# Kernel tuning notes

Hardware: AMD Instinct MI355X
Metric: run time of the kernel (lower is better)

## Reference

```python
import jax, jax.numpy as jnp
import numpy as np

V, K, E, T, B = 30000, 50, 300, 60, 128
TH, H, L = 800, 200, 3
DELTA = 0.005


def setup_inputs():
    key = jax.random.key(0)
    ks = jax.random.split(key, 32)
    n = jax.random.normal
    inp = {}
    inp['bows'] = jax.random.randint(ks[0], (B, V), 0, 5).astype(jnp.float32)
    inp['normalized_bows'] = jax.random.uniform(ks[1], (B, V), jnp.float32)
    inp['times'] = jax.random.randint(ks[2], (B,), 0, T).astype(jnp.int32)
    inp['rnn_inp'] = jax.random.uniform(ks[3], (T, V), jnp.float32)
    inp['num_docs'] = 100000
    inp['eps_alpha'] = n(ks[4], (T, K, E), jnp.float32)
    inp['eps_eta'] = n(ks[5], (T, K), jnp.float32)
    inp['eps_theta'] = n(ks[6], (B, K), jnp.float32)
    # parameters
    inp['rho'] = n(ks[7], (V, E), jnp.float32) * 0.1
    inp['mu_q_alpha'] = n(ks[8], (K, T, E), jnp.float32)
    inp['logsigma_q_alpha'] = n(ks[9], (K, T, E), jnp.float32) * 0.1
    s = lambda d: np.float32(1.0 / np.sqrt(d))
    inp['W1'] = n(ks[10], (TH, V + K), jnp.float32) * s(V + K)
    inp['b1'] = jnp.zeros((TH,), jnp.float32)
    inp['W2'] = n(ks[11], (TH, TH), jnp.float32) * s(TH)
    inp['b2'] = jnp.zeros((TH,), jnp.float32)
    inp['Wmu_t'] = n(ks[12], (K, TH), jnp.float32) * s(TH)
    inp['bmu_t'] = jnp.zeros((K,), jnp.float32)
    inp['Wls_t'] = n(ks[13], (K, TH), jnp.float32) * s(TH)
    inp['bls_t'] = jnp.zeros((K,), jnp.float32)
    inp['Wmap'] = n(ks[14], (H, V), jnp.float32) * s(V)
    inp['bmap'] = jnp.zeros((H,), jnp.float32)
    inp['lstm_Wih'] = n(ks[15], (L, 4 * H, H), jnp.float32) * s(H)
    inp['lstm_Whh'] = n(ks[16], (L, 4 * H, H), jnp.float32) * s(H)
    inp['lstm_bih'] = jnp.zeros((L, 4 * H), jnp.float32)
    inp['lstm_bhh'] = jnp.zeros((L, 4 * H), jnp.float32)
    inp['Wmu_e'] = n(ks[17], (K, H + K), jnp.float32) * s(H + K)
    inp['bmu_e'] = jnp.zeros((K,), jnp.float32)
    inp['Wls_e'] = n(ks[18], (K, H + K), jnp.float32) * s(H + K)
    inp['bls_e'] = jnp.zeros((K,), jnp.float32)
    return inp


def _kl(qm, qls, pm, pls):
    # KL(N(qm, exp(qls)) || N(pm, exp(pls))), summed over last dim (matches torch code)
    return 0.5 * jnp.sum((jnp.exp(qls) + (qm - pm) ** 2) / (jnp.exp(pls) + 1e-6)
                         - 1.0 + pls - qls, axis=-1)


def _lstm_layer(x, Wih, Whh, bih, bhh):
    # x: [T, in]; PyTorch gate order i,f,g,o
    Hh = Whh.shape[1]
    def step(carry, xt):
        h, c = carry
        g = Wih @ xt + bih + Whh @ h + bhh
        i, f, gg, o = jnp.split(g, 4)
        c = jax.nn.sigmoid(f) * c + jax.nn.sigmoid(i) * jnp.tanh(gg)
        h = jax.nn.sigmoid(o) * jnp.tanh(c)
        return (h, c), h
    init = (jnp.zeros((Hh,), x.dtype), jnp.zeros((Hh,), x.dtype))
    _, ys = jax.lax.scan(step, init, x)
    return ys


def reference(bows, normalized_bows, times, rnn_inp, num_docs, eps_alpha, eps_eta,
              eps_theta, rho, mu_q_alpha, logsigma_q_alpha, W1, b1, W2, b2,
              Wmu_t, bmu_t, Wls_t, bls_t, Wmap, bmap, lstm_Wih, lstm_Whh,
              lstm_bih, lstm_bhh, Wmu_e, bmu_e, Wls_e, bls_e):
    nT = mu_q_alpha.shape[1]
    nK = mu_q_alpha.shape[0]
    logdelta = jnp.log(jnp.asarray(DELTA, jnp.float32))
    # ---- get_alpha (vectorized: alphas have no sequential dependence) ----
    mu_a = jnp.transpose(mu_q_alpha, (1, 0, 2))        # [T,K,E]
    ls_a = jnp.transpose(logsigma_q_alpha, (1, 0, 2))  # [T,K,E]
    alphas = mu_a + eps_alpha * jnp.exp(0.5 * ls_a)
    kl_a0 = _kl(mu_a[0], ls_a[0], 0.0, 0.0)                       # [K]
    kl_at = _kl(mu_a[1:], ls_a[1:], alphas[:-1], logdelta)        # [T-1,K]
    kl_alpha = kl_a0.sum() + kl_at.sum()
    # ---- get_eta (sequential chain via scan) ----
    inp_map = rnn_inp @ Wmap.T + bmap                 # [T,H]
    out = inp_map
    for l in range(lstm_Wih.shape[0]):
        out = _lstm_layer(out, lstm_Wih[l], lstm_Whh[l], lstm_bih[l], lstm_bhh[l])
    inp0 = jnp.concatenate([out[0], jnp.zeros((nK,), out.dtype)])
    mu0 = Wmu_e @ inp0 + bmu_e
    ls0 = Wls_e @ inp0 + bls_e
    eta0 = mu0 + eps_eta[0] * jnp.exp(0.5 * ls0)
    kl_e0 = _kl(mu0, ls0, 0.0, 0.0)
    def step(eta_prev, xs):
        out_t, eps_t = xs
        inp_t = jnp.concatenate([out_t, eta_prev])
        mu_t = Wmu_e @ inp_t + bmu_e
        ls_t = Wls_e @ inp_t + bls_e
        eta_t = mu_t + eps_t * jnp.exp(0.5 * ls_t)
        kl_t = _kl(mu_t, ls_t, eta_prev, logdelta)
        return eta_t, (eta_t, kl_t)
    _, (etas_rest, kls) = jax.lax.scan(step, eta0, (out[1:], eps_eta[1:]))
    etas = jnp.concatenate([eta0[None], etas_rest], axis=0)   # [T,K]
    kl_eta = kl_e0 + kls.sum()
    # ---- get_theta ----
    eta_td = etas[times]                                       # [B,K]
    qt_in = jnp.concatenate([normalized_bows, eta_td], axis=1) # [B,V+K]
    h1 = jax.nn.relu(qt_in @ W1.T + b1)
    h2 = jax.nn.relu(h1 @ W2.T + b2)
    mu_th = h2 @ Wmu_t.T + bmu_t
    ls_th = h2 @ Wls_t.T + bls_t
    z = mu_th + eps_theta * jnp.exp(0.5 * ls_th)
    theta = jax.nn.softmax(z, axis=-1)                         # [B,K]
    kl_theta = _kl(mu_th, ls_th, eta_td, 0.0)                  # [B]
    # ---- get_beta / nll ----
    logit = jnp.einsum('tke,ve->tkv', alphas, rho)             # [T,K,V]
    beta = jax.nn.softmax(logit, axis=-1)
    beta_td = beta[times]                                      # [B,K,V]
    loglik = jnp.log(jnp.einsum('bk,bkv->bv', theta, beta_td) + 1e-6)
    nll = (-(loglik * bows)).sum(-1)                           # [B]
    coeff = jnp.asarray(num_docs / bows.shape[0], jnp.float32)
    nll_tot = nll.sum() * coeff
    kl_theta_tot = kl_theta.sum() * coeff
    nelbo = nll_tot + kl_alpha + kl_eta + kl_theta_tot
    return (nelbo, nll_tot, kl_alpha, kl_eta, kl_theta_tot)
```

## Files before the change

### kernel.cpp

```cpp
#include <hip/hip_runtime.h>
#include <hip/hip_fp16.h>
#include <math.h>

#define TID ((int)threadIdx.x)

#define NVB 235
#define NVB2 79

static __device__ __forceinline__ float sigf(float x){ return 1.f/(1.f+expf(-x)); }

static __device__ __forceinline__ unsigned short f2bf(float f){
  unsigned u = __float_as_uint(f);
  unsigned r = (u + 0x7FFFu + ((u>>16)&1u)) >> 16;
  return (unsigned short)r;
}

typedef short v8ss __attribute__((ext_vector_type(8)));
typedef float v16f __attribute__((ext_vector_type(16)));
union I4BF { int4 i; v8ss s; };
union U16B { int4 i; __half2 h2[4]; };

#define REP25(M) M(0) M(1) M(2) M(3) M(4) M(5) M(6) M(7) M(8) M(9) M(10) M(11) \
                 M(12) M(13) M(14) M(15) M(16) M(17) M(18) M(19) M(20) M(21) M(22) M(23) M(24)

#define DECLW(n) int4 w##n = wrow[n];
#define DOTW(n) { U16B u; u.i = w##n; \
    float4 hA = hs4[2*(n)], hB = hs4[2*(n)+1]; \
    float2 q0=__half22float2(u.h2[0]), q1=__half22float2(u.h2[1]); \
    float2 q2=__half22float2(u.h2[2]), q3=__half22float2(u.h2[3]); \
    a0=fmaf(q0.x,hA.x,a0); a1=fmaf(q0.y,hA.y,a1); \
    a2=fmaf(q1.x,hA.z,a2); a3=fmaf(q1.y,hA.w,a3); \
    a0=fmaf(q2.x,hB.x,a0); a1=fmaf(q2.y,hB.y,a1); \
    a2=fmaf(q3.x,hB.z,a2); a3=fmaf(q3.y,hB.w,a3); }

__global__ void k_zero(float* acc, int* flags){
  if (TID<8) acc[TID]=0.f;
  if (TID<160) flags[TID]=0;
}

__global__ void k_alphas(const float* __restrict__ mqa, const float* __restrict__ lqa,
                         const float* __restrict__ eps, float* __restrict__ alphas){
  int i = blockIdx.x*256+TID; if (i>=900000) return;
  int t = i/15000, r = i%15000, k = r/300, e = r%300;
  int src = k*18000 + t*300 + e;
  float mu = mqa[src], ls = lqa[src];
  alphas[i] = mu + eps[i]*expf(0.5f*ls);
}

__global__ void k_klalpha(const float* __restrict__ mqa, const float* __restrict__ lqa,
                          const float* __restrict__ alphas, float* acc){
  __shared__ float red[256];
  int i = blockIdx.x*256+TID;
  float term = 0.f;
  if (i<900000){
    int t = i/15000, r = i%15000, k = r/300, e = r%300;
    int src = k*18000 + t*300 + e;
    float mu = mqa[src], ls = lqa[src];
    if (t==0){
      term = (expf(ls)+mu*mu)*(1.0f/(1.0f+1e-6f)) - 1.f - ls;
    } else {
      float d = mu - alphas[i-15000];
      term = (expf(ls)+d*d)*(1.0f/(0.005f+1e-6f)) - 1.f + logf(0.005f) - ls;
    }
  }
  red[TID]=term; __syncthreads();
  for (int s=128;s>0;s>>=1){ if (TID<s) red[TID]+=red[TID+s]; __syncthreads(); }
  if (TID==0) atomicAdd(acc+0, 0.5f*red[0]);
}

__global__ void k_prep_rho(const float* __restrict__ rho, unsigned short* __restrict__ rho_f){
  int tid = blockIdx.x*256+TID;
  if (tid >= 940*19*64) return;
  int lane = tid & 63;
  int F = tid >> 6;
  int kstep = F % 19;
  int r32 = F / 19;
  int v = r32*32 + (lane & 31);
  int e0 = kstep*16 + ((lane>>5)<<3);
  unsigned short u[8];
  #pragma unroll
  for (int j=0;j<8;j++){
    int e = e0 + j;
    float val = (v < 30000 && e < 300) ? rho[v*300 + e] : 0.f;
    u[j] = f2bf(val);
  }
  int4 o;
  o.x = (int)u[0] | ((int)u[1]<<16);
  o.y = (int)u[2] | ((int)u[3]<<16);
  o.z = (int)u[4] | ((int)u[5]<<16);
  o.w = (int)u[6] | ((int)u[7]<<16);
  ((int4*)rho_f)[tid] = o;
}

__global__ void k_prep_alpha(const float* __restrict__ alphas, unsigned short* __restrict__ alpha_f){
  int tid = blockIdx.x*256+TID;
  if (tid >= 60*2*19*64) return;
  int lane = tid & 63;
  int F = tid >> 6;
  int kstep = F % 19;
  int tn = F / 19;
  int nt = tn % 2, t = tn / 2;
  int k = nt*32 + (lane & 31);
  int e0 = kstep*16 + ((lane>>5)<<3);
  unsigned short u[8];
  #pragma unroll
  for (int j=0;j<8;j++){
    int e = e0 + j;
    float val = (k < 50 && e < 300) ? alphas[t*15000 + k*300 + e] : 0.f;
    u[j] = f2bf(val);
  }
  int4 o;
  o.x = (int)u[0] | ((int)u[1]<<16);
  o.y = (int)u[2] | ((int)u[3]<<16);
  o.z = (int)u[4] | ((int)u[5]<<16);
  o.w = (int)u[6] | ((int)u[7]<<16);
  ((int4*)alpha_f)[tid] = o;
}

__global__ void k_prep_w16(const float* __restrict__ Whh, const float* __restrict__ Wih,
                           __half* __restrict__ WhhH, __half* __restrict__ WihH){
  int i = blockIdx.x*256+TID;
  if (i<480000){
    WhhH[i] = __float2half_rn(Whh[i]);
    WihH[i] = __float2half_rn(Wih[i]);
  }
}

__global__ void k_iminit(float* __restrict__ im, const float* __restrict__ bmap){
  int i = blockIdx.x*256+TID; if (i<12000) im[i] = bmap[i%200];
}

__global__ __launch_bounds__(256,2) void k_imgemm(const float* __restrict__ rnn,
        const float* __restrict__ Wmap, float* __restrict__ im){
  __shared__ __align__(16) float Ws[32*500];
  __shared__ __align__(16) float rnS[500];
  int hb = blockIdx.x;
  int kb = blockIdx.y;
  int h0 = hb*32;
  int nh = (h0+32<=200)?32:(200-h0);
  const int kbase = kb*500;
  for (int i=TID; i<nh*125; i+=256){
    int h = i/125, q = i%125;
    *reinterpret_cast<float4*>(&Ws[h*500 + q*4]) =
      *reinterpret_cast<const float4*>(&Wmap[(h0+h)*30000 + kbase + q*4]);
  }
  int h = TID>>3, sub = TID&7;
  bool act = (h < nh);
  __syncthreads();
  for (int t=0;t<60;t++){
    if (TID<125)
      *reinterpret_cast<float4*>(&rnS[TID*4]) =
        *reinterpret_cast<const float4*>(&rnn[t*30000 + kbase + TID*4]);
    __syncthreads();
    float a = 0.f;
    if (act){
      const float2* wp = reinterpret_cast<const float2*>(&Ws[h*500]);
      const float2* rp = reinterpret_cast<const float2*>(rnS);
      for (int k2=sub;k2<250;k2+=8){
        float2 wv=wp[k2], rv=rp[k2];
        a = fmaf(wv.x,rv.x,a); a = fmaf(wv.y,rv.y,a);
      }
    }
    a += __shfl_down(a,4); a += __shfl_down(a,2); a += __shfl_down(a,1);
    if (act && sub==0) atomicAdd(&im[t*200 + h0 + h], a);
    __syncthreads();
  }
}

__global__ void k_pregates(const float* __restrict__ x, const float* __restrict__ Wih,
                           const float* __restrict__ bih, const float* __restrict__ bhh,
                           float* __restrict__ pre){
  __shared__ float xS[200];
  int t = blockIdx.x;
  if (TID<200) xS[TID] = x[t*200+TID];
  __syncthreads();
  int r = blockIdx.y*256 + TID;
  if (r>=800) return;
  float a = bih[r] + bhh[r];
  const float* wp = Wih + r*200;
  #pragma unroll 4
  for (int c=0;c<200;c++) a = fmaf(wp[c], xS[c], a);
  pre[t*800+r] = a;
}

__global__ void k_h1init(float* __restrict__ h1, const float* __restrict__ b1){
  int i = blockIdx.x*256+TID; if (i<102400) h1[i] = b1[i%800];
}


static __device__ __forceinline__ void pipe_wait(int* flag, int val){
  if (TID==0){
    while (__hip_atomic_load(flag, __ATOMIC_ACQUIRE, __HIP_MEMORY_SCOPE_AGENT) < val)
      __builtin_amdgcn_s_sleep(2);
  }
  __syncthreads();
}

static __device__ __forceinline__ void pipe_post(int* flag, int val){
  if (TID==0)
    __hip_atomic_store(flag, val, __ATOMIC_RELEASE, __HIP_MEMORY_SCOPE_AGENT);
}

static __device__ void lstm_rec(char* sm, const float* __restrict__ pre,
    const __half* __restrict__ WhhH, float* __restrict__ out,
    int* inFlag, int* outFlag)
{
  float* hsF = (float*)sm;
  float* gsh = (float*)(sm + 800);
  __half* wtH = (__half*)(sm + 4000);
  for (int i=TID;i<6400;i+=768) wtH[i] = WhhH[768*200 + i];
  const int4* wrow = reinterpret_cast<const int4*>(WhhH + TID*200);
  REP25(DECLW)
  float c_reg = 0.f;
  if (TID<200) hsF[TID]=0.f;
  int j = TID - 512;
  int trow = (j>=0) ? (j>>3) : 0;
  int tseg = (j>=0) ? (j&7)*25 : 0;
  __syncthreads();
  for (int t=0;t<60;t++){
    if (inFlag) pipe_wait(inFlag, t+1);
    float p = pre[t*800+TID];
    float a0=0.f,a1=0.f,a2=0.f,a3=0.f;
    const float4* hs4 = reinterpret_cast<const float4*>(hsF);
    REP25(DOTW)
    gsh[TID] = a0+a1+a2+a3 + p;
    if (j>=0){
      float pa = 0.f;
      const __half* wt = &wtH[trow*200 + tseg];
      const float* hp = &hsF[tseg];
      #pragma unroll
      for (int c2=0;c2<25;c2++) pa = fmaf(__half2float(wt[c2]), hp[c2], pa);
      pa += __shfl_down(pa,4); pa += __shfl_down(pa,2); pa += __shfl_down(pa,1);
      if ((j&7)==0) gsh[768+trow] = pa + pre[t*800+768+trow];
    }
    __syncthreads();
    if (TID<200){
      float ii=gsh[TID], ff=gsh[200+TID], gg=gsh[400+TID], oo=gsh[600+TID];
      float c = sigf(ff)*c_reg + sigf(ii)*tanhf(gg);
      c_reg = c;
      float h = sigf(oo)*tanhf(c);
      hsF[TID]=h;
      out[t*200+TID]=h;
    }
    __syncthreads();
    if (outFlag) pipe_post(outFlag, t+1);
  }
}

static __device__ void lstm_gemv(char* sm, const float* __restrict__ xIn,
    const __half* __restrict__ WH, const float* __restrict__ bih,
    const float* __restrict__ bhh, float* __restrict__ preOut,
    int* inFlag, int* outFlag)
{
  float* xS = (float*)sm;
  __half* wtG = (__half*)(sm + 800);
  for (int i=TID;i<6400;i+=768) wtG[i] = WH[768*200 + i];
  const int4* wrow = reinterpret_cast<const int4*>(WH + TID*200);
  REP25(DECLW)
  float bb = bih[TID] + bhh[TID];
  int j = TID - 512;
  int trow = (j>=0) ? (j>>3) : 0;
  int tseg = (j>=0) ? (j&7)*25 : 0;
  float bbT = 0.f;
  if (j>=0 && (j&7)==0) bbT = bih[768+trow] + bhh[768+trow];
  for (int t=0;t<60;t++){
    pipe_wait(inFlag, t+1);
    if (TID<200) xS[TID] = xIn[t*200+TID];
    __syncthreads();
    float a0=0.f,a1=0.f,a2=0.f,a3=0.f;
    const float4* hs4 = reinterpret_cast<const float4*>(xS);
    REP25(DOTW)
    preOut[t*800+TID] = a0+a1+a2+a3 + bb;
    if (j>=0){
      float pa = 0.f;
      const __half* wt = &wtG[trow*200 + tseg];
      const float* hp = &xS[tseg];
      #pragma unroll
      for (int c2=0;c2<25;c2++) pa = fmaf(__half2float(wt[c2]), hp[c2], pa);
      pa += __shfl_down(pa,4); pa += __shfl_down(pa,2); pa += __shfl_down(pa,1);
      if ((j&7)==0) preOut[t*800+768+trow] = pa + bbT;
    }
    __syncthreads();
    pipe_post(outFlag, t+1);
  }
}

static __device__ void eta_stage(char* sm, const float* __restrict__ outF,
    const float* __restrict__ Wmu, const float* __restrict__ bmu,
    const float* __restrict__ Wls, const float* __restrict__ bls,
    const float* __restrict__ eps, float* __restrict__ etas, float* acc,
    int* inFlag)
{
  __half* wS = (__half*)sm;
  float* inp = (float*)(sm + 50816);
  float* pt  = (float*)(sm + 51840);
  float* muS = (float*)(sm + 52640);
  float* lsS = (float*)(sm + 52896);
  for (int i=TID;i<12500;i+=768) wS[(i/250)*254 + (i%250)] = __float2half_rn(Wmu[i]);
  for (int i=TID;i<12500;i+=768) wS[(50+i/250)*254 + (i%250)] = __float2half_rn(Wls[i]);
  if (TID<50) inp[200+TID]=0.f;
  const float LOGD = logf(0.005f);
  float kacc = 0.f;
  __syncthreads();
  for (int t=0;t<60;t++){
    pipe_wait(inFlag, t+1);
    if (TID<200) inp[TID] = outF[t*200+TID];
    __syncthreads();
    if (TID<200){
      int rr = TID%100, hf = TID/100;
      const __half* wp = &wS[rr*254 + hf*125];
      const float* ip = &inp[hf*125];
      float s=0.f;
      for (int c=0;c<125;c++) s = fmaf(__half2float(wp[c]), ip[c], s);
      pt[TID]=s;
    }
    __syncthreads();
    if (TID<100){
      float v = pt[TID]+pt[TID+100];
      if (TID<50) muS[TID] = v + bmu[TID];
      else lsS[TID-50] = v + bls[TID-50];
    }
    __syncthreads();
    if (TID<64){
      float term=0.f;
      if (TID<50){
        float mu=muS[TID], ls=lsS[TID], ep=inp[200+TID];
        if (t==0) term = (expf(ls)+mu*mu)*(1.0f/(1.0f+1e-6f)) - 1.f - ls;
        else { float d=mu-ep; term = (expf(ls)+d*d)*(1.0f/(0.005f+1e-6f)) - 1.f + LOGD - ls; }
        float et = mu + eps[t*50+TID]*expf(0.5f*ls);
        etas[t*50+TID]=et;
        inp[200+TID]=et;
      }
      for (int o=32;o>0;o>>=1) term += __shfl_down(term,o);
      if (TID==0) kacc += 0.5f*term;
    }
    __syncthreads();
  }
  if (TID==0) atomicAdd(acc+1, kacc);
}

static __device__ void mf1_block(char* sm, int vb, int tg,
    const unsigned short* __restrict__ rho_f, const unsigned short* __restrict__ alpha_f,
    float* __restrict__ Mp, float* __restrict__ Sp)
{
  float* redM = (float*)sm;
  float* redS = (float*)(sm + 3072);
  int wid = TID>>6, lane = TID&63;
  int r32 = vb*12 + wid;
  bool valid = (r32 < 940);
  int4 zi; zi.x=0; zi.y=0; zi.z=0; zi.w=0;
  const int4* ap = ((const int4*)rho_f) + (r32*19)*64 + lane;
  int4 a[19];
  #pragma unroll
  for (int ks=0;ks<19;ks++) a[ks] = valid ? ap[ks*64] : zi;
  int rowbase = vb*384 + wid*32 + ((lane>>5)<<2);
  for (int t = tg*15; t < tg*15+15; t++){
    v16f acc0, acc1;
    #pragma unroll
    for (int i=0;i<16;i++){ acc0[i]=0.f; acc1[i]=0.f; }
    const int4* bp = ((const int4*)alpha_f) + (t*38)*64 + lane;
    #pragma unroll
    for (int ks=0;ks<19;ks++){
      I4BF av, b0, b1;
      av.i = a[ks];
      b0.i = bp[ks*64];
      b1.i = bp[(19+ks)*64];
      acc0 = __builtin_amdgcn_mfma_f32_32x32x16_bf16(av.s, b0.s, acc0, 0,0,0);
      acc1 = __builtin_amdgcn_mfma_f32_32x32x16_bf16(av.s, b1.s, acc1, 0,0,0);
    }
    float m0=-INFINITY, m1=-INFINITY;
    #pragma unroll
    for (int r=0;r<16;r++){
      int v = rowbase + (r&3) + ((r>>2)<<3);
      if (v < 30000){ m0 = fmaxf(m0, acc0[r]); m1 = fmaxf(m1, acc1[r]); }
    }
    m0 = fmaxf(m0, __shfl_xor(m0, 32));
    m1 = fmaxf(m1, __shfl_xor(m1, 32));
    float s0=0.f, s1=0.f;
    #pragma unroll
    for (int r=0;r<16;r++){
      int v = rowbase + (r&3) + ((r>>2)<<3);
      if (v < 30000){ s0 += expf(acc0[r]-m0); s1 += expf(acc1[r]-m1); }
    }
    s0 += __shfl_xor(s0, 32);
    s1 += __shfl_xor(s1, 32);
    if (lane < 32){
      redM[wid*64+lane] = m0; redM[wid*64+lane+32] = m1;
      redS[wid*64+lane] = s0; redS[wid*64+lane+32] = s1;
    }
    __syncthreads();
    if (TID < 50){
      float M = redM[TID];
      #pragma unroll
      for (int w2=1; w2<12; w2++) M = fmaxf(M, redM[w2*64+TID]);
      float S = 0.f;
      #pragma unroll
      for (int w2=0; w2<12; w2++){
        float mw = redM[w2*64+TID];
        if (mw > -INFINITY) S += redS[w2*64+TID] * expf(mw - M);
      }
      Mp[(t*50+TID)*NVB2 + vb] = M;
      Sp[(t*50+TID)*NVB2 + vb] = S;
    }
    __syncthreads();
  }
}

static __device__ void h1_block(char* sm, int rtg, int sp,
    const float* __restrict__ nb, const float* __restrict__ W1,
    float* __restrict__ h1)
{
  float* As = (float*)sm;
  float* WsAll = (float*)(sm + 8448);
  int sub = TID>>8, l = TID&255;
  int rt = rtg*3 + sub;
  float* Ws = WsAll + sub*(16*68);
  int kbeg = sp*940;
  int kend = kbeg+940; if (kend>30000) kend=30000;
  int b0 = (l%32)*4, r0 = (l/32)*8;
  float acc[32];
  #pragma unroll
  for (int jj=0;jj<32;jj++) acc[jj]=0.f;
  for (int kb=kbeg; kb<kend; kb+=16){
    __syncthreads();
    for (int i=TID;i<2048;i+=768){
      int b=i>>4, kk=i&15, kg=kb+kk;
      As[kk*132+b] = (kg<kend) ? nb[b*30000+kg] : 0.f;
    }
    for (int i=l;i<1024;i+=256){
      int r=i>>4, kk=i&15, kg=kb+kk, rg=rt*64+r;
      Ws[kk*68+r] = (kg<kend && rg<800) ? W1[rg*30050+kg] : 0.f;
    }
    __syncthreads();
    #pragma unroll
    for (int kk=0;kk<16;kk++){
      float4 a4 = *reinterpret_cast<const float4*>(&As[kk*132+b0]);
      float4 w4 = *reinterpret_cast<const float4*>(&Ws[kk*68+r0]);
      float4 w5 = *reinterpret_cast<const float4*>(&Ws[kk*68+r0+4]);
      float aa[4]={a4.x,a4.y,a4.z,a4.w};
      float ww[8]={w4.x,w4.y,w4.z,w4.w,w5.x,w5.y,w5.z,w5.w};
      #pragma unroll
      for (int j=0;j<4;j++)
        #pragma unroll
        for (int i2=0;i2<8;i2++) acc[j*8+i2] = fmaf(aa[j], ww[i2], acc[j*8+i2]);
    }
  }
  #pragma unroll
  for (int j=0;j<4;j++){
    int b=b0+j;
    #pragma unroll
    for (int i2=0;i2<8;i2++){
      int rg = rt*64+r0+i2;
      if (rg<800) atomicAdd(&h1[b*800+rg], acc[j*8+i2]);
    }
  }
}

__global__ __launch_bounds__(768,3) void k_mega(
    const float* __restrict__ pre0, const __half* __restrict__ WhhH,
    const __half* __restrict__ WihH, const float* __restrict__ bih,
    const float* __restrict__ bhh, float* __restrict__ out0,
    float* __restrict__ out1, float* __restrict__ out2,
    float* __restrict__ pre1, float* __restrict__ pre2, int* __restrict__ flags,
    const float* __restrict__ Wmu_e, const float* __restrict__ bmu_e,
    const float* __restrict__ Wls_e, const float* __restrict__ bls_e,
    const float* __restrict__ eps_e, float* __restrict__ etas, float* acc,
    const unsigned short* __restrict__ rho_f, const unsigned short* __restrict__ alpha_f,
    float* __restrict__ Mp, float* __restrict__ Sp,
    const float* __restrict__ nb, const float* __restrict__ W1, float* __restrict__ h1)
{
  __shared__ __align__(16) unsigned char smem[53248];
  char* sm = (char*)smem;
  int bid = blockIdx.x;
  if (bid==0)      lstm_rec (sm, pre0, WhhH,        out0, nullptr,   flags+0);
  else if (bid==1) lstm_gemv(sm, out0, WihH+160000, bih+800,  bhh+800,  pre1, flags+0,  flags+32);
  else if (bid==2) lstm_rec (sm, pre1, WhhH+160000, out1, flags+32, flags+64);
  else if (bid==3) lstm_gemv(sm, out1, WihH+320000, bih+1600, bhh+1600, pre2, flags+64, flags+96);
  else if (bid==4) lstm_rec (sm, pre2, WhhH+320000, out2, flags+96, flags+128);
  else if (bid==5) eta_stage(sm, out2, Wmu_e, bmu_e, Wls_e, bls_e, eps_e, etas, acc, flags+128);
  else if (bid<322){ int i=bid-6;   mf1_block(sm, i>>2, i&3, rho_f, alpha_f, Mp, Sp); }
  else             { int j=bid-322; h1_block(sm, j>>5, j&31, nb, W1, h1); }
}

__global__ void k_h1eta(const float* __restrict__ etas, const int* __restrict__ times,
                        const float* __restrict__ W1, float* __restrict__ h1){
  __shared__ float eS[50];
  int b = blockIdx.x;
  if (TID<50) eS[TID] = etas[times[b]*50 + TID];
  __syncthreads();
  for (int r=TID; r<800; r+=256){
    const float* wp = W1 + r*30050 + 30000;
    float a2=0.f;
    #pragma unroll 10
    for (int c=0;c<50;c++) a2 = fmaf(wp[c], eS[c], a2);
    h1[b*800+r] += a2;
  }
}

__global__ void k_msred(const float* __restrict__ Mp, const float* __restrict__ Sp,
                        float* __restrict__ Mg, float* __restrict__ iSg){
  __shared__ float red[256];
  int row = blockIdx.x;
  float m = (TID<NVB2) ? Mp[row*NVB2+TID] : -INFINITY;
  red[TID]=m; __syncthreads();
  for (int s=128;s>0;s>>=1){ if (TID<s) red[TID]=fmaxf(red[TID],red[TID+s]); __syncthreads(); }
  float M = red[0]; __syncthreads();
  float sv = (TID<NVB2) ? Sp[row*NVB2+TID]*expf(m-M) : 0.f;
  red[TID]=sv; __syncthreads();
  for (int s=128;s>0;s>>=1){ if (TID<s) red[TID]+=red[TID+s]; __syncthreads(); }
  if (TID==0){ Mg[row]=M; iSg[row]=1.f/red[0]; }
}

__global__ __launch_bounds__(256) void k_h2(const float* __restrict__ h1,
        const float* __restrict__ W2, const float* __restrict__ b2,
        float* __restrict__ h2){
  __shared__ __align__(16) float As[16*33];
  __shared__ __align__(16) float Ws[16*68];
  int bt = blockIdx.x;
  int rt = blockIdx.y;
  int b0 = (TID%16)*2, r0 = (TID/16)*4;
  float acc[8] = {0,0,0,0,0,0,0,0};
  for (int kb=0; kb<800; kb+=16){
    __syncthreads();
    for (int i=TID;i<512;i+=256){
      int b=i>>4, k=i&15;
      As[k*33+b] = fmaxf(h1[(bt*32+b)*800 + kb + k], 0.f);
    }
    for (int i=TID;i<1024;i+=256){
      int r=i>>4, k=i&15; int rg = rt*64+r;
      Ws[k*68+r] = (rg<800) ? W2[rg*800 + kb + k] : 0.f;
    }
    __syncthreads();
    #pragma unroll
    for (int k=0;k<16;k++){
      float a0=As[k*33+b0], a1=As[k*33+b0+1];
      float4 w4 = *reinterpret_cast<const float4*>(&Ws[k*68+r0]);
      acc[0]=fmaf(a0,w4.x,acc[0]); acc[1]=fmaf(a0,w4.y,acc[1]);
      acc[2]=fmaf(a0,w4.z,acc[2]); acc[3]=fmaf(a0,w4.w,acc[3]);
      acc[4]=fmaf(a1,w4.x,acc[4]); acc[5]=fmaf(a1,w4.y,acc[5]);
      acc[6]=fmaf(a1,w4.z,acc[6]); acc[7]=fmaf(a1,w4.w,acc[7]);
    }
  }
  #pragma unroll
  for (int jj=0;jj<2;jj++){
    int b = bt*32 + b0 + jj;
    #pragma unroll
    for (int i2=0;i2<4;i2++){
      int rg = rt*64 + r0 + i2;
      if (rg<800) h2[b*800+rg] = fmaxf(acc[jj*4+i2] + b2[rg], 0.f);
    }
  }
}

__global__ void k_muls(const float* __restrict__ h2, const float* __restrict__ Wmu,
                       const float* __restrict__ bmu, const float* __restrict__ Wls,
                       const float* __restrict__ bls, float* __restrict__ muth,
                       float* __restrict__ lsth){
  __shared__ float hS[800];
  int b = blockIdx.x;
  for (int i=TID;i<800;i+=128) hS[i] = h2[b*800+i];
  __syncthreads();
  if (TID<50){
    float a = bmu[TID];
    const float* wp = Wmu + TID*800;
    #pragma unroll 4
    for (int c=0;c<800;c++) a = fmaf(wp[c], hS[c], a);
    muth[b*50+TID]=a;
  } else if (TID>=64 && TID<114){
    int r = TID-64;
    float a = bls[r];
    const float* wp = Wls + r*800;
    #pragma unroll 4
    for (int c=0;c<800;c++) a = fmaf(wp[c], hS[c], a);
    lsth[b*50+r]=a;
  }
}

__global__ void k_theta(const float* __restrict__ muth, const float* __restrict__ lsth,
                        const float* __restrict__ etas, const int* __restrict__ times,
                        const float* __restrict__ epsth, float* __restrict__ theta,
                        float* acc){
  int b = blockIdx.x, k = TID;
  bool a = k<50;
  int tb = times[b];
  float mu=0.f, ls=0.f, etd=0.f, z=-INFINITY;
  if (a){
    mu = muth[b*50+k]; ls = lsth[b*50+k]; etd = etas[tb*50+k];
    z = mu + epsth[b*50+k]*expf(0.5f*ls);
  }
  float m=z;
  for (int o=32;o>0;o>>=1) m = fmaxf(m, __shfl_xor(m,o));
  float e = a ? expf(z-m) : 0.f;
  float s = e;
  for (int o=32;o>0;o>>=1) s += __shfl_xor(s,o);
  if (a) theta[b*50+k] = e/s;
  float term = a ? ((expf(ls)+(mu-etd)*(mu-etd))*(1.0f/(1.0f+1e-6f)) - 1.f - ls) : 0.f;
  for (int o=32;o>0;o>>=1) term += __shfl_xor(term,o);
  if (TID==0) atomicAdd(acc+2, 0.5f*term);
}

__global__ __launch_bounds__(256,2) void k_mf2(const unsigned short* __restrict__ rho_f,
        const unsigned short* __restrict__ alpha_f,
        const float* __restrict__ Mg, const float* __restrict__ iSg,
        const float* __restrict__ theta, const int* __restrict__ times,
        const float* __restrict__ bows, float* acc){
  __shared__ float thS[128*52];
  __shared__ float tileS[4][32*66];
  __shared__ int tS[128];
  __shared__ int cntS[64];
  int vb = blockIdx.x, tg = blockIdx.y;
  int wid = TID>>6, lane = TID&63;
  if (TID < 64) cntS[TID] = 0;
  __syncthreads();
  if (TID < 128){ int tv = times[TID]; tS[TID] = tv; atomicAdd(&cntS[tv], 1); }
  for (int i=TID; i<6400; i+=256){ int b=i/50, c=i%50; thS[b*52+c] = theta[i]; }
  int r32 = vb*4 + wid;
  const int4* ap = ((const int4*)rho_f) + (r32*19)*64 + lane;
  int4 a[19];
  #pragma unroll
  for (int ks=0;ks<19;ks++) a[ks] = ap[ks*64];
  __syncthreads();
  float local = 0.f;
  int rb32 = ((lane>>5)<<2);
  int c0 = lane&31, c1 = 32 + (lane&31);
  for (int t = tg*15; t < tg*15+15; t++){
    if (cntS[t] == 0) continue;
    v16f acc0, acc1;
    #pragma unroll
    for (int i=0;i<16;i++){ acc0[i]=0.f; acc1[i]=0.f; }
    const int4* bp = ((const int4*)alpha_f) + (t*38)*64 + lane;
    #pragma unroll
    for (int ks=0;ks<19;ks++){
      I4BF av, b0, b1;
      av.i = a[ks];
      b0.i = bp[ks*64];
      b1.i = bp[(19+ks)*64];
      acc0 = __builtin_amdgcn_mfma_f32_32x32x16_bf16(av.s, b0.s, acc0, 0,0,0);
      acc1 = __builtin_amdgcn_mfma_f32_32x32x16_bf16(av.s, b1.s, acc1, 0,0,0);
    }
    float M0 = Mg[t*50+c0], i0 = iSg[t*50+c0];
    float M1 = 0.f, i1 = 0.f;
    if (c1 < 50){ M1 = Mg[t*50+c1]; i1 = iSg[t*50+c1]; }
    float* tl = &tileS[wid][0];
    #pragma unroll
    for (int r=0;r<16;r++){
      int row = rb32 + (r&3) + ((r>>2)<<3);
      tl[row*66 + c0] = expf(acc0[r]-M0)*i0;
      if (c1 < 50) tl[row*66 + c1] = expf(acc1[r]-M1)*i1;
    }
    __syncthreads();
    for (int b=0;b<128;b++){
      if (tS[b] != t) continue;
      int row = lane&31;
      int v = vb*128 + wid*32 + row;
      const float* th = &thS[b*52 + (lane>>5)*25];
      const float* tp = &tl[row*66 + (lane>>5)*25];
      float mix = 0.f;
      #pragma unroll 5
      for (int c=0;c<25;c++) mix = fmaf(th[c], tp[c], mix);
      mix += __shfl_xor(mix, 32);
      if (lane < 32 && v < 30000)
        local -= logf(mix + 1e-6f) * bows[b*30000 + v];
    }
    __syncthreads();
  }
  for (int o=1;o<64;o<<=1) local += __shfl_xor(local, o);
  if (lane==0) atomicAdd(acc+3, local);
}

__global__ void k_final(const float* __restrict__ acc, const int* __restrict__ nd,
                        float* __restrict__ out){
  float coeff = (float)(*nd) / 128.0f;
  float nll = acc[3]*coeff;
  float klth = acc[2]*coeff;
  out[0] = nll + acc[0] + acc[1] + klth;
  out[1] = nll;
  out[2] = acc[0];
  out[3] = acc[1];
  out[4] = klth;
}

extern "C" void kernel_launch(void* const* d_in, const int* in_sizes, int n_in,
                              void* d_out, int out_size, void* d_ws, size_t ws_size,
                              hipStream_t stream) {
  (void)in_sizes; (void)n_in; (void)out_size; (void)ws_size;
  const float* bows  = (const float*)d_in[0];
  const float* nb    = (const float*)d_in[1];
  const int*   times = (const int*)d_in[2];
  const float* rnn   = (const float*)d_in[3];
  const int*   ndocs = (const int*)d_in[4];
  const float* eps_a = (const float*)d_in[5];
  const float* eps_e = (const float*)d_in[6];
  const float* eps_t = (const float*)d_in[7];
  const float* rho   = (const float*)d_in[8];
  const float* mqa   = (const float*)d_in[9];
  const float* lqa   = (const float*)d_in[10];
  const float* W1    = (const float*)d_in[11];
  const float* b1    = (const float*)d_in[12];
  const float* W2    = (const float*)d_in[13];
  const float* b2    = (const float*)d_in[14];
  const float* Wmu_t = (const float*)d_in[15];
  const float* bmu_t = (const float*)d_in[16];
  const float* Wls_t = (const float*)d_in[17];
  const float* bls_t = (const float*)d_in[18];
  const float* Wmap  = (const float*)d_in[19];
  const float* bmap  = (const float*)d_in[20];
  const float* Wih   = (const float*)d_in[21];
  const float* Whh   = (const float*)d_in[22];
  const float* bih   = (const float*)d_in[23];
  const float* bhh   = (const float*)d_in[24];
  const float* Wmu_e = (const float*)d_in[25];
  const float* bmu_e = (const float*)d_in[26];
  const float* Wls_e = (const float*)d_in[27];
  const float* bls_e = (const float*)d_in[28];
  float* out = (float*)d_out;

  float* p = (float*)d_ws;
  float* acc    = p; p += 8;
  unsigned short* rho_f   = (unsigned short*)p; p += 4572160;
  unsigned short* alpha_f = (unsigned short*)p; p += 583680;
  float* alphas = p; p += 900000;
  float* im     = p; p += 12000;
  float* out0   = p; p += 12000;
  float* out1   = p; p += 12000;
  float* out2   = p; p += 12000;
  float* pre0   = p; p += 48000;
  float* pre1   = p; p += 48000;
  float* pre2   = p; p += 48000;
  float* etas   = p; p += 3000;
  float* h1     = p; p += 102400;
  float* h2     = p; p += 102400;
  float* muth   = p; p += 6400;
  float* lsth   = p; p += 6400;
  float* theta  = p; p += 6400;
  float* Mp     = p; p += 3000*NVB2;
  float* Sp     = p; p += 3000*NVB2;
  float* Mg     = p; p += 3000;
  float* iSg    = p; p += 3000;
  __half* whhH  = (__half*)p; p += 240000;
  __half* wihH  = (__half*)p; p += 240000;
  int*   flags  = (int*)p; p += 256;

  k_zero<<<1,256,0,stream>>>(acc, flags);
  k_alphas<<<3516,256,0,stream>>>(mqa, lqa, eps_a, alphas);
  k_klalpha<<<3516,256,0,stream>>>(mqa, lqa, alphas, acc);
  k_prep_rho<<<4465,256,0,stream>>>(rho, rho_f);
  k_prep_alpha<<<570,256,0,stream>>>(alphas, alpha_f);
  k_prep_w16<<<1875,256,0,stream>>>(Whh, Wih, whhH, wihH);
  k_iminit<<<47,256,0,stream>>>(im, bmap);
  k_imgemm<<<dim3(7,60),256,0,stream>>>(rnn, Wmap, im);
  k_pregates<<<dim3(60,4),256,0,stream>>>(im, Wih, bih, bhh, pre0);
  k_h1init<<<400,256,0,stream>>>(h1, b1);

  k_mega<<<482,768,0,stream>>>(pre0, whhH, wihH, bih, bhh, out0, out1, out2,
                               pre1, pre2, flags,
                               Wmu_e, bmu_e, Wls_e, bls_e, eps_e, etas, acc,
                               rho_f, alpha_f, Mp, Sp, nb, W1, h1);

  k_msred<<<3000,256,0,stream>>>(Mp, Sp, Mg, iSg);
  k_h1eta<<<128,256,0,stream>>>(etas, times, W1, h1);
  k_h2<<<dim3(4,13),256,0,stream>>>(h1, W2, b2, h2);
  k_muls<<<128,128,0,stream>>>(h2, Wmu_t, bmu_t, Wls_t, bls_t, muth, lsth);
  k_theta<<<128,64,0,stream>>>(muth, lsth, etas, times, eps_t, theta, acc);
  k_mf2<<<dim3(NVB,4),256,0,stream>>>(rho_f, alpha_f, Mg, iSg, theta, times, bows, acc);
  k_final<<<1,1,0,stream>>>(acc, ndocs, out);
}
```

Before: 1.615 ms.

## Fold prep and tail kernels into persistent megakernel with flag-based dataflow

Several launches are removed. The alpha and KL-alpha kernels merge into one. Rho bf16 packing moves into the mf1 blocks, and fp16 weight conversion moves into the LSTM blocks. The msred, h1eta, h2, muls and theta stages become extra roles in the megakernel, gated by atomic counters, and the final reduction moves into the last k_mf2 block. The mf1 blocks are halved in count with a doubled time range, and tanh, exp and log use fast intrinsics. This cuts launch gaps and serialization, but relies on all 403 blocks of 768 threads being co-resident to avoid deadlock, and trades some accuracy for speed.

Result: slower. 1.688 ms (+4.5%).

```diff
diff --git a/kernel.cpp b/kernel.cpp
--- a/kernel.cpp
+++ b/kernel.cpp
@@ -7,7 +7,25 @@
 #define NVB 235
 #define NVB2 79
 
-static __device__ __forceinline__ float sigf(float x){ return 1.f/(1.f+expf(-x)); }
+#define FG_S01   0
+#define FG_S12   32
+#define FG_S23   64
+#define FG_S34   96
+#define FG_S45   128
+#define FG_ETAT  160
+#define FG_MF1D  192
+#define FG_H1D   196
+#define FG_H1ED  200
+#define FG_H2D   204
+#define FG_MULSD 208
+#define FG_MF2D  212
+
+static __device__ __forceinline__ float sigf(float x){ return 1.f/(1.f+__expf(-x)); }
+static __device__ __forceinline__ float tanhfast(float x){
+  float t = fminf(fmaxf(x,-15.f),15.f);
+  float e = __expf(2.f*t);
+  return (e-1.f)/(e+1.f);
+}
 
 static __device__ __forceinline__ unsigned short f2bf(float f){
   unsigned u = __float_as_uint(f);
@@ -23,7 +41,10 @@
 #define REP25(M) M(0) M(1) M(2) M(3) M(4) M(5) M(6) M(7) M(8) M(9) M(10) M(11) \
                  M(12) M(13) M(14) M(15) M(16) M(17) M(18) M(19) M(20) M(21) M(22) M(23) M(24)
 
-#define DECLW(n) int4 w##n = wrow[n];
+#define DECLWF(n) int4 w##n; { float4 fA = rowF[2*(n)], fB = rowF[2*(n)+1]; U16B u; \
+    u.h2[0]=__floats2half2_rn(fA.x,fA.y); u.h2[1]=__floats2half2_rn(fA.z,fA.w); \
+    u.h2[2]=__floats2half2_rn(fB.x,fB.y); u.h2[3]=__floats2half2_rn(fB.z,fB.w); w##n=u.i; }
+
 #define DOTW(n) { U16B u; u.i = w##n; \
     float4 hA = hs4[2*(n)], hB = hs4[2*(n)+1]; \
     float2 q0=__half22float2(u.h2[0]), q1=__half22float2(u.h2[1]); \
@@ -35,20 +56,12 @@
 
 __global__ void k_zero(float* acc, int* flags){
   if (TID<8) acc[TID]=0.f;
-  if (TID<160) flags[TID]=0;
-}
-
-__global__ void k_alphas(const float* __restrict__ mqa, const float* __restrict__ lqa,
-                         const float* __restrict__ eps, float* __restrict__ alphas){
-  int i = blockIdx.x*256+TID; if (i>=900000) return;
-  int t = i/15000, r = i%15000, k = r/300, e = r%300;
-  int src = k*18000 + t*300 + e;
-  float mu = mqa[src], ls = lqa[src];
-  alphas[i] = mu + eps[i]*expf(0.5f*ls);
-}
-
-__global__ void k_klalpha(const float* __restrict__ mqa, const float* __restrict__ lqa,
-                          const float* __restrict__ alphas, float* acc){
+  if (TID<256) flags[TID]=0;
+}
+
+__global__ void k_alphakl(const float* __restrict__ mqa, const float* __restrict__ lqa,
+                          const float* __restrict__ eps, float* __restrict__ alphas,
+                          float* acc){
   __shared__ float red[256];
   int i = blockIdx.x*256+TID;
   float term = 0.f;
@@ -56,40 +69,20 @@
     int t = i/15000, r = i%15000, k = r/300, e = r%300;
     int src = k*18000 + t*300 + e;
     float mu = mqa[src], ls = lqa[src];
+    alphas[i] = mu + eps[i]*__expf(0.5f*ls);
     if (t==0){
-      term = (expf(ls)+mu*mu)*(1.0f/(1.0f+1e-6f)) - 1.f - ls;
+      term = (__expf(ls)+mu*mu)*(1.0f/(1.0f+1e-6f)) - 1.f - ls;
     } else {
-      float d = mu - alphas[i-15000];
-      term = (expf(ls)+d*d)*(1.0f/(0.005f+1e-6f)) - 1.f + logf(0.005f) - ls;
+      int sp = src - 300;
+      float mup = mqa[sp], lsp = lqa[sp];
+      float ap = mup + eps[i-15000]*__expf(0.5f*lsp);
+      float d = mu - ap;
+      term = (__expf(ls)+d*d)*(1.0f/(0.005f+1e-6f)) - 1.f + logf(0.005f) - ls;
     }
   }
   red[TID]=term; __syncthreads();
   for (int s=128;s>0;s>>=1){ if (TID<s) red[TID]+=red[TID+s]; __syncthreads(); }
   if (TID==0) atomicAdd(acc+0, 0.5f*red[0]);
-}
-
-__global__ void k_prep_rho(const float* __restrict__ rho, unsigned short* __restrict__ rho_f){
-  int tid = blockIdx.x*256+TID;
-  if (tid >= 940*19*64) return;
-  int lane = tid & 63;
-  int F = tid >> 6;
-  int kstep = F % 19;
-  int r32 = F / 19;
-  int v = r32*32 + (lane & 31);
-  int e0 = kstep*16 + ((lane>>5)<<3);
-  unsigned short u[8];
-  #pragma unroll
-  for (int j=0;j<8;j++){
-    int e = e0 + j;
-    float val = (v < 30000 && e < 300) ? rho[v*300 + e] : 0.f;
-    u[j] = f2bf(val);
-  }
-  int4 o;
-  o.x = (int)u[0] | ((int)u[1]<<16);
-  o.y = (int)u[2] | ((int)u[3]<<16);
-  o.z = (int)u[4] | ((int)u[5]<<16);
-  o.w = (int)u[6] | ((int)u[7]<<16);
-  ((int4*)rho_f)[tid] = o;
 }
 
 __global__ void k_prep_alpha(const float* __restrict__ alphas, unsigned short* __restrict__ alpha_f){
@@ -117,15 +110,6 @@
   ((int4*)alpha_f)[tid] = o;
 }
 
-__global__ void k_prep_w16(const float* __restrict__ Whh, const float* __restrict__ Wih,
-                           __half* __restrict__ WhhH, __half* __restrict__ WihH){
-  int i = blockIdx.x*256+TID;
-  if (i<480000){
-    WhhH[i] = __float2half_rn(Whh[i]);
-    WihH[i] = __float2half_rn(Wih[i]);
-  }
-}
-
 __global__ void k_iminit(float* __restrict__ im, const float* __restrict__ bmap){
   int i = blockIdx.x*256+TID; if (i<12000) im[i] = bmap[i%200];
 }
@@ -183,15 +167,13 @@
   pre[t*800+r] = a;
 }
 
-__global__ void k_h1init(float* __restrict__ h1, const float* __restrict__ b1){
-  int i = blockIdx.x*256+TID; if (i<102400) h1[i] = b1[i%800];
-}
-
-
+
+template<int SLP>
 static __device__ __forceinline__ void pipe_wait(int* flag, int val){
   if (TID==0){
-    while (__hip_atomic_load(flag, __ATOMIC_ACQUIRE, __HIP_MEMORY_SCOPE_AGENT) < val)
-      __builtin_amdgcn_s_sleep(2);
+    while (__hip_atomic_load(flag, __ATOMIC_RELAXED, __HIP_MEMORY_SCOPE_AGENT) < val)
+      __builtin_amdgcn_s_sleep(SLP);
+    (void)__hip_atomic_load(flag, __ATOMIC_ACQUIRE, __HIP_MEMORY_SCOPE_AGENT);
   }
   __syncthreads();
 }
@@ -201,16 +183,22 @@
     __hip_atomic_store(flag, val, __ATOMIC_RELEASE, __HIP_MEMORY_SCOPE_AGENT);
 }
 
+static __device__ __forceinline__ void post_done(int* ctr){
+  __syncthreads();
+  if (TID==0)
+    __hip_atomic_fetch_add(ctr, 1, __ATOMIC_RELEASE, __HIP_MEMORY_SCOPE_AGENT);
+}
+
 static __device__ void lstm_rec(char* sm, const float* __restrict__ pre,
-    const __half* __restrict__ WhhH, float* __restrict__ out,
+    const float* __restrict__ WhhF, float* __restrict__ out,
     int* inFlag, int* outFlag)
 {
   float* hsF = (float*)sm;
   float* gsh = (float*)(sm + 800);
   __half* wtH = (__half*)(sm + 4000);
-  for (int i=TID;i<6400;i+=768) wtH[i] = WhhH[768*200 + i];
-  const int4* wrow = reinterpret_cast<const int4*>(WhhH + TID*200);
-  REP25(DECLW)
+  for (int i=TID;i<6400;i+=768) wtH[i] = __float2half_rn(WhhF[768*200 + i]);
+  const float4* rowF = reinterpret_cast<const float4*>(WhhF + TID*200);
+  REP25(DECLWF)
   float c_reg = 0.f;
   if (TID<200) hsF[TID]=0.f;
   int j = TID - 512;
@@ -218,7 +206,7 @@
   int tseg = (j>=0) ? (j&7)*25 : 0;
   __syncthreads();
   for (int t=0;t<60;t++){
-    if (inFlag) pipe_wait(inFlag, t+1);
+    if (inFlag) pipe_wait<1>(inFlag, t+1);
     float p = pre[t*800+TID];
     float a0=0.f,a1=0.f,a2=0.f,a3=0.f;
     const float4* hs4 = reinterpret_cast<const float4*>(hsF);
@@ -236,9 +224,9 @@
     __syncthreads();
     if (TID<200){
       float ii=gsh[TID], ff=gsh[200+TID], gg=gsh[400+TID], oo=gsh[600+TID];
-      float c = sigf(ff)*c_reg + sigf(ii)*tanhf(gg);
+      float c = sigf(ff)*c_reg + sigf(ii)*tanhfast(gg);
       c_reg = c;
-      float h = sigf(oo)*tanhf(c);
+      float h = sigf(oo)*tanhfast(c);
       hsF[TID]=h;
       out[t*200+TID]=h;
     }
@@ -248,15 +236,15 @@
 }
 
 static __device__ void lstm_gemv(char* sm, const float* __restrict__ xIn,
-    const __half* __restrict__ WH, const float* __restrict__ bih,
+    const float* __restrict__ WF, const float* __restrict__ bih,
     const float* __restrict__ bhh, float* __restrict__ preOut,
     int* inFlag, int* outFlag)
 {
   float* xS = (float*)sm;
   __half* wtG = (__half*)(sm + 800);
-  for (int i=TID;i<6400;i+=768) wtG[i] = WH[768*200 + i];
-  const int4* wrow = reinterpret_cast<const int4*>(WH + TID*200);
-  REP25(DECLW)
+  for (int i=TID;i<6400;i+=768) wtG[i] = __float2half_rn(WF[768*200 + i]);
+  const float4* rowF = reinterpret_cast<const float4*>(WF + TID*200);
+  REP25(DECLWF)
   float bb = bih[TID] + bhh[TID];
   int j = TID - 512;
   int trow = (j>=0) ? (j>>3) : 0;
@@ -264,7 +252,7 @@
   float bbT = 0.f;
   if (j>=0 && (j&7)==0) bbT = bih[768+trow] + bhh[768+trow];
   for (int t=0;t<60;t++){
-    pipe_wait(inFlag, t+1);
+    pipe_wait<1>(inFlag, t+1);
     if (TID<200) xS[TID] = xIn[t*200+TID];
     __syncthreads();
     float a0=0.f,a1=0.f,a2=0.f,a3=0.f;
@@ -289,7 +277,7 @@
     const float* __restrict__ Wmu, const float* __restrict__ bmu,
     const float* __restrict__ Wls, const float* __restrict__ bls,
     const float* __restrict__ eps, float* __restrict__ etas, float* acc,
-    int* inFlag)
+    int* inFlag, int* etaT)
 {
   __half* wS = (__half*)sm;
   float* inp = (float*)(sm + 50816);
@@ -303,7 +291,7 @@
   float kacc = 0.f;
   __syncthreads();
   for (int t=0;t<60;t++){
-    pipe_wait(inFlag, t+1);
+    pipe_wait<1>(inFlag, t+1);
     if (TID<200) inp[TID] = outF[t*200+TID];
     __syncthreads();
     if (TID<200){
@@ -325,9 +313,9 @@
       float term=0.f;
       if (TID<50){
         float mu=muS[TID], ls=lsS[TID], ep=inp[200+TID];
-        if (t==0) term = (expf(ls)+mu*mu)*(1.0f/(1.0f+1e-6f)) - 1.f - ls;
-        else { float d=mu-ep; term = (expf(ls)+d*d)*(1.0f/(0.005f+1e-6f)) - 1.f + LOGD - ls; }
-        float et = mu + eps[t*50+TID]*expf(0.5f*ls);
+        if (t==0) term = (__expf(ls)+mu*mu)*(1.0f/(1.0f+1e-6f)) - 1.f - ls;
+        else { float d=mu-ep; term = (__expf(ls)+d*d)*(1.0f/(0.005f+1e-6f)) - 1.f + LOGD - ls; }
+        float et = mu + eps[t*50+TID]*__expf(0.5f*ls);
         etas[t*50+TID]=et;
         inp[200+TID]=et;
       }
@@ -335,14 +323,40 @@
       if (TID==0) kacc += 0.5f*term;
     }
     __syncthreads();
+    pipe_post(etaT, t+1);
   }
   if (TID==0) atomicAdd(acc+1, kacc);
 }
 
 static __device__ void mf1_block(char* sm, int vb, int tg,
-    const unsigned short* __restrict__ rho_f, const unsigned short* __restrict__ alpha_f,
-    float* __restrict__ Mp, float* __restrict__ Sp)
-{
+    const float* __restrict__ rho,
+    unsigned short* __restrict__ rho_f, const unsigned short* __restrict__ alpha_f,
+    float* __restrict__ Mp, float* __restrict__ Sp, int* mf1d)
+{
+  for (int i=TID; i<12*19*64; i+=768){
+    int lane2 = i & 63;
+    int F = i >> 6;
+    int kstep = F % 19;
+    int rr = F / 19;
+    int r32p = vb*12 + rr;
+    if (r32p >= 940) continue;
+    int v = r32p*32 + (lane2 & 31);
+    int e0 = kstep*16 + ((lane2>>5)<<3);
+    unsigned short u[8];
+    #pragma unroll
+    for (int jj=0;jj<8;jj++){
+      int e = e0 + jj;
+      float val = (v < 30000 && e < 300) ? rho[v*300 + e] : 0.f;
+      u[jj] = f2bf(val);
+    }
+    int4 o;
+    o.x = (int)u[0] | ((int)u[1]<<16);
+    o.y = (int)u[2] | ((int)u[3]<<16);
+    o.z = (int)u[4] | ((int)u[5]<<16);
+    o.w = (int)u[6] | ((int)u[7]<<16);
+    ((int4*)rho_f)[(r32p*19 + kstep)*64 + lane2] = o;
+  }
+  __syncthreads();
   float* redM = (float*)sm;
   float* redS = (float*)(sm + 3072);
   int wid = TID>>6, lane = TID&63;
@@ -354,7 +368,7 @@
   #pragma unroll
   for (int ks=0;ks<19;ks++) a[ks] = valid ? ap[ks*64] : zi;
   int rowbase = vb*384 + wid*32 + ((lane>>5)<<2);
-  for (int t = tg*15; t < tg*15+15; t++){
+  for (int t = tg*30; t < tg*30+30; t++){
     v16f acc0, acc1;
     #pragma unroll
     for (int i=0;i<16;i++){ acc0[i]=0.f; acc1[i]=0.f; }
@@ -380,7 +394,7 @@
     #pragma unroll
     for (int r=0;r<16;r++){
       int v = rowbase + (r&3) + ((r>>2)<<3);
-      if (v < 30000){ s0 += expf(acc0[r]-m0); s1 += expf(acc1[r]-m1); }
+      if (v < 30000){ s0 += __expf(acc0[r]-m0); s1 += __expf(acc1[r]-m1); }
     }
     s0 += __shfl_xor(s0, 32);
     s1 += __shfl_xor(s1, 32);
@@ -397,18 +411,19 @@
       #pragma unroll
       for (int w2=0; w2<12; w2++){
         float mw = redM[w2*64+TID];
-        if (mw > -INFINITY) S += redS[w2*64+TID] * expf(mw - M);
+        if (mw > -INFINITY) S += redS[w2*64+TID] * __expf(mw - M);
       }
       Mp[(t*50+TID)*NVB2 + vb] = M;
       Sp[(t*50+TID)*NVB2 + vb] = S;
     }
     __syncthreads();
   }
+  post_done(mf1d);
 }
 
 static __device__ void h1_block(char* sm, int rtg, int sp,
     const float* __restrict__ nb, const float* __restrict__ W1,
-    float* __restrict__ h1)
+    float* __restrict__ h1, int* h1d)
 {
   float* As = (float*)sm;
   float* WsAll = (float*)(sm + 8448);
@@ -454,156 +469,211 @@
       if (rg<800) atomicAdd(&h1[b*800+rg], acc[j*8+i2]);
     }
   }
+  post_done(h1d);
+}
+
+static __device__ void msred_role(int blk, const float* __restrict__ Mp,
+    const float* __restrict__ Sp, float* __restrict__ Mg, float* __restrict__ iSg,
+    int* mf1d)
+{
+  pipe_wait<16>(mf1d, 158);
+  int w = TID>>6, lane = TID&63;
+  for (int row = blk*12 + w; row < 3000; row += 144){
+    float m0 = (lane < NVB2) ? Mp[row*NVB2 + lane] : -INFINITY;
+    float m1 = (64+lane < NVB2) ? Mp[row*NVB2 + 64 + lane] : -INFINITY;
+    float s0 = (lane < NVB2) ? Sp[row*NVB2 + lane] : 0.f;
+    float s1 = (64+lane < NVB2) ? Sp[row*NVB2 + 64 + lane] : 0.f;
+    float mm = fmaxf(m0, m1);
+    for (int o=32;o>0;o>>=1) mm = fmaxf(mm, __shfl_xor(mm,o));
+    float e = 0.f;
+    if (m0 > -INFINITY) e += s0*__expf(m0-mm);
+    if (m1 > -INFINITY) e += s1*__expf(m1-mm);
+    for (int o=32;o>0;o>>=1) e += __shfl_xor(e,o);
+    if (lane==0){ Mg[row]=mm; iSg[row]=1.f/e; }
+  }
+}
+
+static __device__ void h1eta_role(char* sm, int blk, const float* __restrict__ etas,
+    const int* __restrict__ times, const float* __restrict__ W1,
+    const float* __restrict__ b1, float* __restrict__ h1, int* etaT, int* h1ed)
+{
+  float* eS = (float*)sm;
+  for (int d=0; d<8; d++){
+    int b = blk*8 + d;
+    int tb = times[b];
+    pipe_wait<4>(etaT, tb+1);
+    if (TID<50) eS[TID] = etas[tb*50+TID];
+    __syncthreads();
+    for (int r=TID; r<800; r+=768){
+      const float* wp = W1 + r*30050 + 30000;
+      float a2 = b1[r];
+      #pragma unroll 10
+      for (int c=0;c<50;c++) a2 = fmaf(wp[c], eS[c], a2);
+      atomicAdd(&h1[b*800+r], a2);
+    }
+    __syncthreads();
+  }
+  post_done(h1ed);
+}
+
+static __device__ void h2_role(char* sm, int blk, const float* __restrict__ h1,
+    const float* __restrict__ W2, const float* __restrict__ b2,
+    float* __restrict__ h2, int* h1d, int* h1ed, int* h2d)
+{
+  pipe_wait<16>(h1d, 160);
+  pipe_wait<16>(h1ed, 16);
+  int sub = TID>>8, l = TID&255;
+  int tile = blk*3 + sub;
+  bool tv = (tile < 52);
+  int bt = tile/13, rt = tile%13;
+  float* As = (float*)sm + sub*(16*33);
+  float* Ws = (float*)(sm + 3*16*33*4) + sub*(16*68);
+  int b0 = (l%16)*2, r0 = (l/16)*4;
+  float acc[8] = {0,0,0,0,0,0,0,0};
+  for (int kb=0; kb<800; kb+=16){
+    __syncthreads();
+    if (tv){
+      for (int i=l;i<512;i+=256){
+        int b=i>>4, k=i&15;
+        As[k*33+b] = fmaxf(h1[(bt*32+b)*800 + kb + k], 0.f);
+      }
+      for (int i=l;i<1024;i+=256){
+        int r=i>>4, k=i&15; int rg = rt*64+r;
+        Ws[k*68+r] = (rg<800) ? W2[rg*800 + kb + k] : 0.f;
+      }
+    }
+    __syncthreads();
+    if (tv){
+      #pragma unroll
+      for (int k=0;k<16;k++){
+        float a0=As[k*33+b0], a1=As[k*33+b0+1];
+        float4 w4 = *reinterpret_cast<const float4*>(&Ws[k*68+r0]);
+        acc[0]=fmaf(a0,w4.x,acc[0]); acc[1]=fmaf(a0,w4.y,acc[1]);
+        acc[2]=fmaf(a0,w4.z,acc[2]); acc[3]=fmaf(a0,w4.w,acc[3]);
+        acc[4]=fmaf(a1,w4.x,acc[4]); acc[5]=fmaf(a1,w4.y,acc[5]);
+        acc[6]=fmaf(a1,w4.z,acc[6]); acc[7]=fmaf(a1,w4.w,acc[7]);
+      }
+    }
+  }
+  if (tv){
+    #pragma unroll
+    for (int jj=0;jj<2;jj++){
+      int b = bt*32 + b0 + jj;
+      #pragma unroll
+      for (int i2=0;i2<4;i2++){
+        int rg = rt*64 + r0 + i2;
+        if (rg<800) h2[b*800+rg] = fmaxf(acc[jj*4+i2] + b2[rg], 0.f);
+      }
+    }
+  }
+  post_done(h2d);
+}
+
+static __device__ void muls_role(char* sm, int blk, const float* __restrict__ h2,
+    const float* __restrict__ Wmu, const float* __restrict__ bmu,
+    const float* __restrict__ Wls, const float* __restrict__ bls,
+    float* __restrict__ muth, float* __restrict__ lsth, int* h2d, int* mulsd)
+{
+  pipe_wait<16>(h2d, 18);
+  int sd = TID>>7, l = TID&127;
+  int b = blk*6 + sd;
+  bool bv = (b < 128);
+  float* hS = (float*)sm + sd*800;
+  if (bv){ for (int i=l;i<800;i+=128) hS[i] = h2[b*800+i]; }
+  __syncthreads();
+  if (bv){
+    if (l<50){
+      float a = bmu[l];
+      const float* wp = Wmu + l*800;
+      #pragma unroll 4
+      for (int c=0;c<800;c++) a = fmaf(wp[c], hS[c], a);
+      muth[b*50+l]=a;
+    } else if (l>=64 && l<114){
+      int r = l-64;
+      float a = bls[r];
+      const float* wp = Wls + r*800;
+      #pragma unroll 4
+      for (int c=0;c<800;c++) a = fmaf(wp[c], hS[c], a);
+      lsth[b*50+r]=a;
+    }
+  }
+  post_done(mulsd);
+}
+
+static __device__ void theta_role(int blk, const float* __restrict__ muth,
+    const float* __restrict__ lsth, const float* __restrict__ etas,
+    const int* __restrict__ times, const float* __restrict__ epsth,
+    float* __restrict__ theta, float* acc, int* mulsd)
+{
+  pipe_wait<16>(mulsd, 22);
+  int d = blk*12 + (TID>>6);
+  int k = TID&63;
+  if (d >= 128) return;
+  bool a = k<50;
+  int tb = times[d];
+  float mu=0.f, ls=0.f, etd=0.f, z=-INFINITY;
+  if (a){
+    mu = muth[d*50+k]; ls = lsth[d*50+k]; etd = etas[tb*50+k];
+    z = mu + epsth[d*50+k]*__expf(0.5f*ls);
+  }
+  float m=z;
+  for (int o=32;o>0;o>>=1) m = fmaxf(m, __shfl_xor(m,o));
+  float e = a ? __expf(z-m) : 0.f;
+  float s = e;
+  for (int o=32;o>0;o>>=1) s += __shfl_xor(s,o);
+  if (a) theta[d*50+k] = e/s;
+  float term = a ? ((__expf(ls)+(mu-etd)*(mu-etd))*(1.0f/(1.0f+1e-6f)) - 1.f - ls) : 0.f;
+  for (int o=32;o>0;o>>=1) term += __shfl_xor(term,o);
+  if (k==0) atomicAdd(acc+2, 0.5f*term);
 }
 
 __global__ __launch_bounds__(768,3) void k_mega(
-    const float* __restrict__ pre0, const __half* __restrict__ WhhH,
-    const __half* __restrict__ WihH, const float* __restrict__ bih,
+    const float* __restrict__ pre0, const float* __restrict__ Whh,
+    const float* __restrict__ Wih, const float* __restrict__ bih,
     const float* __restrict__ bhh, float* __restrict__ out0,
     float* __restrict__ out1, float* __restrict__ out2,
     float* __restrict__ pre1, float* __restrict__ pre2, int* __restrict__ flags,
     const float* __restrict__ Wmu_e, const float* __restrict__ bmu_e,
     const float* __restrict__ Wls_e, const float* __restrict__ bls_e,
     const float* __restrict__ eps_e, float* __restrict__ etas, float* acc,
-    const unsigned short* __restrict__ rho_f, const unsigned short* __restrict__ alpha_f,
+    const float* __restrict__ rho, unsigned short* __restrict__ rho_f,
+    const unsigned short* __restrict__ alpha_f,
     float* __restrict__ Mp, float* __restrict__ Sp,
-    const float* __restrict__ nb, const float* __restrict__ W1, float* __restrict__ h1)
+    const float* __restrict__ nb, const float* __restrict__ W1,
+    const float* __restrict__ b1, float* __restrict__ h1,
+    const int* __restrict__ times, float* __restrict__ Mg, float* __restrict__ iSg,
+    const float* __restrict__ W2, const float* __restrict__ b2, float* __restrict__ h2,
+    const float* __restrict__ Wmu_t, const float* __restrict__ bmu_t,
+    const float* __restrict__ Wls_t, const float* __restrict__ bls_t,
+    float* __restrict__ muth, float* __restrict__ lsth,
+    const float* __restrict__ eps_t, float* __restrict__ theta)
 {
   __shared__ __align__(16) unsigned char smem[53248];
   char* sm = (char*)smem;
   int bid = blockIdx.x;
-  if (bid==0)      lstm_rec (sm, pre0, WhhH,        out0, nullptr,   flags+0);
-  else if (bid==1) lstm_gemv(sm, out0, WihH+160000, bih+800,  bhh+800,  pre1, flags+0,  flags+32);
-  else if (bid==2) lstm_rec (sm, pre1, WhhH+160000, out1, flags+32, flags+64);
-  else if (bid==3) lstm_gemv(sm, out1, WihH+320000, bih+1600, bhh+1600, pre2, flags+64, flags+96);
-  else if (bid==4) lstm_rec (sm, pre2, WhhH+320000, out2, flags+96, flags+128);
-  else if (bid==5) eta_stage(sm, out2, Wmu_e, bmu_e, Wls_e, bls_e, eps_e, etas, acc, flags+128);
-  else if (bid<322){ int i=bid-6;   mf1_block(sm, i>>2, i&3, rho_f, alpha_f, Mp, Sp); }
-  else             { int j=bid-322; h1_block(sm, j>>5, j&31, nb, W1, h1); }
-}
-
-__global__ void k_h1eta(const float* __restrict__ etas, const int* __restrict__ times,
-                        const float* __restrict__ W1, float* __restrict__ h1){
-  __shared__ float eS[50];
-  int b = blockIdx.x;
-  if (TID<50) eS[TID] = etas[times[b]*50 + TID];
-  __syncthreads();
-  for (int r=TID; r<800; r+=256){
-    const float* wp = W1 + r*30050 + 30000;
-    float a2=0.f;
-    #pragma unroll 10
-    for (int c=0;c<50;c++) a2 = fmaf(wp[c], eS[c], a2);
-    h1[b*800+r] += a2;
-  }
-}
-
-__global__ void k_msred(const float* __restrict__ Mp, const float* __restrict__ Sp,
-                        float* __restrict__ Mg, float* __restrict__ iSg){
-  __shared__ float red[256];
-  int row = blockIdx.x;
-  float m = (TID<NVB2) ? Mp[row*NVB2+TID] : -INFINITY;
-  red[TID]=m; __syncthreads();
-  for (int s=128;s>0;s>>=1){ if (TID<s) red[TID]=fmaxf(red[TID],red[TID+s]); __syncthreads(); }
-  float M = red[0]; __syncthreads();
-  float sv = (TID<NVB2) ? Sp[row*NVB2+TID]*expf(m-M) : 0.f;
-  red[TID]=sv; __syncthreads();
-  for (int s=128;s>0;s>>=1){ if (TID<s) red[TID]+=red[TID+s]; __syncthreads(); }
-  if (TID==0){ Mg[row]=M; iSg[row]=1.f/red[0]; }
-}
-
-__global__ __launch_bounds__(256) void k_h2(const float* __restrict__ h1,
-        const float* __restrict__ W2, const float* __restrict__ b2,
-        float* __restrict__ h2){
-  __shared__ __align__(16) float As[16*33];
-  __shared__ __align__(16) float Ws[16*68];
-  int bt = blockIdx.x;
-  int rt = blockIdx.y;
-  int b0 = (TID%16)*2, r0 = (TID/16)*4;
-  float acc[8] = {0,0,0,0,0,0,0,0};
-  for (int kb=0; kb<800; kb+=16){
-    __syncthreads();
-    for (int i=TID;i<512;i+=256){
-      int b=i>>4, k=i&15;
-      As[k*33+b] = fmaxf(h1[(bt*32+b)*800 + kb + k], 0.f);
-    }
-    for (int i=TID;i<1024;i+=256){
-      int r=i>>4, k=i&15; int rg = rt*64+r;
-      Ws[k*68+r] = (rg<800) ? W2[rg*800 + kb + k] : 0.f;
-    }
-    __syncthreads();
-    #pragma unroll
-    for (int k=0;k<16;k++){
-      float a0=As[k*33+b0], a1=As[k*33+b0+1];
-      float4 w4 = *reinterpret_cast<const float4*>(&Ws[k*68+r0]);
-      acc[0]=fmaf(a0,w4.x,acc[0]); acc[1]=fmaf(a0,w4.y,acc[1]);
-      acc[2]=fmaf(a0,w4.z,acc[2]); acc[3]=fmaf(a0,w4.w,acc[3]);
-      acc[4]=fmaf(a1,w4.x,acc[4]); acc[5]=fmaf(a1,w4.y,acc[5]);
-      acc[6]=fmaf(a1,w4.z,acc[6]); acc[7]=fmaf(a1,w4.w,acc[7]);
-    }
-  }
-  #pragma unroll
-  for (int jj=0;jj<2;jj++){
-    int b = bt*32 + b0 + jj;
-    #pragma unroll
-    for (int i2=0;i2<4;i2++){
-      int rg = rt*64 + r0 + i2;
-      if (rg<800) h2[b*800+rg] = fmaxf(acc[jj*4+i2] + b2[rg], 0.f);
-    }
-  }
-}
-
-__global__ void k_muls(const float* __restrict__ h2, const float* __restrict__ Wmu,
-                       const float* __restrict__ bmu, const float* __restrict__ Wls,
-                       const float* __restrict__ bls, float* __restrict__ muth,
-                       float* __restrict__ lsth){
-  __shared__ float hS[800];
-  int b = blockIdx.x;
-  for (int i=TID;i<800;i+=128) hS[i] = h2[b*800+i];
-  __syncthreads();
-  if (TID<50){
-    float a = bmu[TID];
-    const float* wp = Wmu + TID*800;
-    #pragma unroll 4
-    for (int c=0;c<800;c++) a = fmaf(wp[c], hS[c], a);
-    muth[b*50+TID]=a;
-  } else if (TID>=64 && TID<114){
-    int r = TID-64;
-    float a = bls[r];
-    const float* wp = Wls + r*800;
-    #pragma unroll 4
-    for (int c=0;c<800;c++) a = fmaf(wp[c], hS[c], a);
-    lsth[b*50+r]=a;
-  }
-}
-
-__global__ void k_theta(const float* __restrict__ muth, const float* __restrict__ lsth,
-                        const float* __restrict__ etas, const int* __restrict__ times,
-                        const float* __restrict__ epsth, float* __restrict__ theta,
-                        float* acc){
-  int b = blockIdx.x, k = TID;
-  bool a = k<50;
-  int tb = times[b];
-  float mu=0.f, ls=0.f, etd=0.f, z=-INFINITY;
-  if (a){
-    mu = muth[b*50+k]; ls = lsth[b*50+k]; etd = etas[tb*50+k];
-    z = mu + epsth[b*50+k]*expf(0.5f*ls);
-  }
-  float m=z;
-  for (int o=32;o>0;o>>=1) m = fmaxf(m, __shfl_xor(m,o));
-  float e = a ? expf(z-m) : 0.f;
-  float s = e;
-  for (int o=32;o>0;o>>=1) s += __shfl_xor(s,o);
-  if (a) theta[b*50+k] = e/s;
-  float term = a ? ((expf(ls)+(mu-etd)*(mu-etd))*(1.0f/(1.0f+1e-6f)) - 1.f - ls) : 0.f;
-  for (int o=32;o>0;o>>=1) term += __shfl_xor(term,o);
-  if (TID==0) atomicAdd(acc+2, 0.5f*term);
+  if (bid==0)      lstm_rec (sm, pre0, Whh,        out0, nullptr,   flags+FG_S01);
+  else if (bid==1) lstm_gemv(sm, out0, Wih+160000, bih+800,  bhh+800,  pre1, flags+FG_S01, flags+FG_S12);
+  else if (bid==2) lstm_rec (sm, pre1, Whh+160000, out1, flags+FG_S12, flags+FG_S23);
+  else if (bid==3) lstm_gemv(sm, out1, Wih+320000, bih+1600, bhh+1600, pre2, flags+FG_S23, flags+FG_S34);
+  else if (bid==4) lstm_rec (sm, pre2, Whh+320000, out2, flags+FG_S34, flags+FG_S45);
+  else if (bid==5) eta_stage(sm, out2, Wmu_e, bmu_e, Wls_e, bls_e, eps_e, etas, acc,
+                             flags+FG_S45, flags+FG_ETAT);
+  else if (bid<164){ int i=bid-6;   mf1_block(sm, i>>1, i&1, rho, rho_f, alpha_f, Mp, Sp, flags+FG_MF1D); }
+  else if (bid<324){ int j=bid-164; h1_block(sm, j>>5, j&31, nb, W1, h1, flags+FG_H1D); }
+  else if (bid<336){ msred_role(bid-324, Mp, Sp, Mg, iSg, flags+FG_MF1D); }
+  else if (bid<352){ h1eta_role(sm, bid-336, etas, times, W1, b1, h1, flags+FG_ETAT, flags+FG_H1ED); }
+  else if (bid<370){ h2_role(sm, bid-352, h1, W2, b2, h2, flags+FG_H1D, flags+FG_H1ED, flags+FG_H2D); }
+  else if (bid<392){ muls_role(sm, bid-370, h2, Wmu_t, bmu_t, Wls_t, bls_t, muth, lsth,
+                               flags+FG_H2D, flags+FG_MULSD); }
+  else             { theta_role(bid-392, muth, lsth, etas, times, eps_t, theta, acc, flags+FG_MULSD); }
 }
 
 __global__ __launch_bounds__(256,2) void k_mf2(const unsigned short* __restrict__ rho_f,
         const unsigned short* __restrict__ alpha_f,
         const float* __restrict__ Mg, const float* __restrict__ iSg,
         const float* __restrict__ theta, const int* __restrict__ times,
-        const float* __restrict__ bows, float* acc){
+        const float* __restrict__ bows, float* acc,
+        const int* __restrict__ nd, float* __restrict__ out, int* __restrict__ flags){
   __shared__ float thS[128*52];
   __shared__ float tileS[4][32*66];
   __shared__ int tS[128];
@@ -645,8 +715,8 @@
     #pragma unroll
     for (int r=0;r<16;r++){
       int row = rb32 + (r&3) + ((r>>2)<<3);
-      tl[row*66 + c0] = expf(acc0[r]-M0)*i0;
-      if (c1 < 50) tl[row*66 + c1] = expf(acc1[r]-M1)*i1;
+      tl[row*66 + c0] = __expf(acc0[r]-M0)*i0;
+      if (c1 < 50) tl[row*66 + c1] = __expf(acc1[r]-M1)*i1;
     }
     __syncthreads();
     for (int b=0;b<128;b++){
@@ -660,24 +730,26 @@
       for (int c=0;c<25;c++) mix = fmaf(th[c], tp[c], mix);
       mix += __shfl_xor(mix, 32);
       if (lane < 32 && v < 30000)
-        local -= logf(mix + 1e-6f) * bows[b*30000 + v];
+        local -= __logf(mix + 1e-6f) * bows[b*30000 + v];
     }
     __syncthreads();
   }
   for (int o=1;o<64;o<<=1) local += __shfl_xor(local, o);
   if (lane==0) atomicAdd(acc+3, local);
-}
-
-__global__ void k_final(const float* __restrict__ acc, const int* __restrict__ nd,
-                        float* __restrict__ out){
-  float coeff = (float)(*nd) / 128.0f;
-  float nll = acc[3]*coeff;
-  float klth = acc[2]*coeff;
-  out[0] = nll + acc[0] + acc[1] + klth;
-  out[1] = nll;
-  out[2] = acc[0];
-  out[3] = acc[1];
-  out[4] = klth;
+  __syncthreads();
+  if (TID==0){
+    int n = __hip_atomic_fetch_add(flags+FG_MF2D, 1, __ATOMIC_ACQ_REL, __HIP_MEMORY_SCOPE_AGENT);
+    if (n == 4*NVB-1){
+      float coeff = (float)(*nd) / 128.0f;
+      float nll = acc[3]*coeff;
+      float klth = acc[2]*coeff;
+      out[0] = nll + acc[0] + acc[1] + klth;
+      out[1] = nll;
+      out[2] = acc[0];
+      out[3] = acc[1];
+      out[4] = klth;
+    }
+  }
 }
 
 extern "C" void kernel_launch(void* const* d_in, const int* in_sizes, int n_in,
@@ -737,31 +809,24 @@
   float* Sp     = p; p += 3000*NVB2;
   float* Mg     = p; p += 3000;
   float* iSg    = p; p += 3000;
-  __half* whhH  = (__half*)p; p += 240000;
-  __half* wihH  = (__half*)p; p += 240000;
   int*   flags  = (int*)p; p += 256;
 
   k_zero<<<1,256,0,stream>>>(acc, flags);
-  k_alphas<<<3516,256,0,stream>>>(mqa, lqa, eps_a, alphas);
-  k_klalpha<<<3516,256,0,stream>>>(mqa, lqa, alphas, acc);
-  k_prep_rho<<<4465,256,0,stream>>>(rho, rho_f);
+  (void)hipMemsetAsync(h1, 0, 102400*sizeof(float), stream);
+  k_alphakl<<<3516,256,0,stream>>>(mqa, lqa, eps_a, alphas, acc);
   k_prep_alpha<<<570,256,0,stream>>>(alphas, alpha_f);
-  k_prep_w16<<<1875,256,0,stream>>>(Whh, Wih, whhH, wihH);
   k_iminit<<<47,256,0,stream>>>(im, bmap);
   k_imgemm<<<dim3(7,60),256,0,stream>>>(rnn, Wmap, im);
   k_pregates<<<dim3(60,4),256,0,stream>>>(im, Wih, bih, bhh, pre0);
-  k_h1init<<<400,256,0,stream>>>(h1, b1);
-
-  k_mega<<<482,768,0,stream>>>(pre0, whhH, wihH, bih, bhh, out0, out1, out2,
+
+  k_mega<<<403,768,0,stream>>>(pre0, Whh, Wih, bih, bhh, out0, out1, out2,
                                pre1, pre2, flags,
                                Wmu_e, bmu_e, Wls_e, bls_e, eps_e, etas, acc,
-                               rho_f, alpha_f, Mp, Sp, nb, W1, h1);
-
-  k_msred<<<3000,256,0,stream>>>(Mp, Sp, Mg, iSg);
-  k_h1eta<<<128,256,0,stream>>>(etas, times, W1, h1);
-  k_h2<<<dim3(4,13),256,0,stream>>>(h1, W2, b2, h2);
-  k_muls<<<128,128,0,stream>>>(h2, Wmu_t, bmu_t, Wls_t, bls_t, muth, lsth);
-  k_theta<<<128,64,0,stream>>>(muth, lsth, etas, times, eps_t, theta, acc);
-  k_mf2<<<dim3(NVB,4),256,0,stream>>>(rho_f, alpha_f, Mg, iSg, theta, times, bows, acc);
-  k_final<<<1,1,0,stream>>>(acc, ndocs, out);
-}
+                               rho, rho_f, alpha_f, Mp, Sp,
+                               nb, W1, b1, h1, times, Mg, iSg,
+                               W2, b2, h2, Wmu_t, bmu_t, Wls_t, bls_t,
+                               muth, lsth, eps_t, theta);
+
+  k_mf2<<<dim3(NVB,4),256,0,stream>>>(rho_f, alpha_f, Mg, iSg, theta, times, bows, acc,
+                                      ndocs, out, flags);
+}
```
